# Kernel optimization log

Measured on AMD Instinct MI355X. Metric: run time of the kernel, lower is better.

Reference implementation:

```python
import jax, jax.numpy as jnp
import numpy as np

N_NODES = 50000
N_EDGES = 800000
IN_CH = 128
OUT_CH = 128


def setup_inputs() -> dict:
    key = jax.random.key(0)
    ks = jax.random.split(key, 8)
    x = jax.random.normal(ks[0], (N_NODES, IN_CH), dtype=jnp.float32)
    edge_index = jax.random.randint(ks[1], (2, N_EDGES), 0, N_NODES, dtype=jnp.int64)
    edge_weight = jax.random.uniform(ks[2], (N_EDGES,), dtype=jnp.float32)
    bound = 1.0 / np.sqrt(IN_CH)
    weight = jax.random.uniform(ks[3], (IN_CH, OUT_CH), minval=-bound, maxval=bound, dtype=jnp.float32)
    lin1_w = jax.random.uniform(ks[4], (OUT_CH, IN_CH), minval=-bound, maxval=bound, dtype=jnp.float32)
    lin1_b = jax.random.uniform(ks[5], (OUT_CH,), minval=-bound, maxval=bound, dtype=jnp.float32)
    lin2_w = jax.random.uniform(ks[6], (OUT_CH, IN_CH), minval=-bound, maxval=bound, dtype=jnp.float32)
    lin2_b = jax.random.uniform(ks[7], (OUT_CH,), minval=-bound, maxval=bound, dtype=jnp.float32)
    return {"x": x, "edge_index": edge_index, "edge_weight": edge_weight,
            "weight": weight, "lin1_w": lin1_w, "lin1_b": lin1_b,
            "lin2_w": lin2_w, "lin2_b": lin2_b}


def reference(x, edge_index, edge_weight, weight, lin1_w, lin1_b, lin2_w, lin2_b):
    num_nodes = x.shape[0]
    row, col = edge_index[0], edge_index[1]
    # remove_self_loops: zero out self-loop edge weights (equivalent math)
    ew = jnp.where(row == col, jnp.zeros((), x.dtype), edge_weight)
    h = x @ weight                                   # [N, out]
    deg = jax.ops.segment_sum(ew, row, num_segments=num_nodes)       # [N]
    h_j = ew[:, None] * h[col]                       # [E, out] gather + weight
    aggr_out = jax.ops.segment_sum(h_j, row, num_segments=num_nodes) # [N, out] scatter-add
    out = deg[:, None] * (x @ lin1_w.T + lin1_b) + aggr_out + (x @ lin2_w.T + lin2_b)
    return out
```

## Files before the change

kernel.cpp:

```cpp
#include <hip/hip_runtime.h>
#include <hip/hip_bf16.h>
#include <hip/hip_fp8.h>

#define NNODES 50000
#define NEDGES 800000
#define CH 128
#define NPAD 50176
#define NPART 256
#define RPP 196
#define PCAP 4096
#define BM 128

#define EPB1 4096
#define NB_PART ((NEDGES + EPB1 - 1) / EPB1)
#define BPS 200

#define NB_PREP 6250
#define NB_WCAT 256

typedef __attribute__((ext_vector_type(8))) short s8;
typedef __attribute__((ext_vector_type(4))) float f32x4;

__device__ inline unsigned pack_edge(int col, float w) {
    unsigned wb = __float_as_uint(w);
    return ((unsigned)col << 16) | ((wb + 0x4000u) >> 15);
}
__device__ inline float unpack_w(unsigned u) {
    return __uint_as_float((u & 0xFFFFu) << 15);
}

__global__ __launch_bounds__(256) void k_pre(const float* __restrict__ x,
                                             unsigned short* __restrict__ xb,
                                             unsigned char* __restrict__ xq,
                                             const float* __restrict__ weight,
                                             const float* __restrict__ l1,
                                             const float* __restrict__ l2,
                                             unsigned short* __restrict__ w1t,
                                             unsigned short* __restrict__ w2t,
                                             const int* __restrict__ ei,
                                             const float* __restrict__ ew,
                                             int* __restrict__ blkpack,
                                             int2* __restrict__ part) {
    const int blk = blockIdx.x;
    const int tid = threadIdx.x;
    if (blk < NB_PART) {
        __shared__ int hist[NPART];
        __shared__ int scn[NPART];
        __shared__ int wsum[4];
        __shared__ int2 stage[EPB1];
        const int lane = tid & 63, wid = tid >> 6;
        hist[tid] = 0;
        __syncthreads();
        const int e0 = blk * EPB1 + tid;
        int rows[16], cols[16], prt[16], rnk[16];
        float wv[16];
#pragma unroll
        for (int j = 0; j < 16; ++j) {
            int e = e0 + j * 256;
            bool v = (e < NEDGES);
            int ee = v ? e : 0;
            rows[j] = v ? ei[ee] : -1;
            cols[j] = ei[NEDGES + ee];
            wv[j] = ew[ee];
        }
#pragma unroll
        for (int j = 0; j < 16; ++j) {
            if (rows[j] >= 0) {
                prt[j] = rows[j] / RPP;
                rnk[j] = atomicAdd(&hist[prt[j]], 1);
            }
        }
        __syncthreads();
        int h = hist[tid];
        int s = h;
#pragma unroll
        for (int off = 1; off < 64; off <<= 1) {
            int u = __shfl_up(s, off);
            if (lane >= off) s += u;
        }
        if (lane == 63) wsum[wid] = s;
        __syncthreads();
        int base = 0;
#pragma unroll
        for (int w = 0; w < 4; ++w) if (w < wid) base += wsum[w];
        int excl = base + s - h;
        blkpack[tid * BPS + blk] = (excl << 13) | h;
        scn[tid] = excl;
        __syncthreads();
#pragma unroll
        for (int j = 0; j < 16; ++j) {
            if (rows[j] < 0) continue;
            int rl = rows[j] - prt[j] * RPP;
            float w = (rows[j] == cols[j]) ? 0.f : wv[j];
            stage[scn[prt[j]] + rnk[j]] =
                make_int2((rl << 16) | cols[j], __float_as_int(w));
        }
        __syncthreads();
        const int nblk = (NEDGES - blk * EPB1 < EPB1) ? (NEDGES - blk * EPB1) : EPB1;
        int2* dst = part + (size_t)blk * EPB1;
        for (int i = tid; i < nblk; i += 256) dst[i] = stage[i];
    } else if (blk < NB_PART + NB_PREP) {
        int g = (blk - NB_PART) * 256 + tid;
        float4 v = ((const float4*)x)[g];
        ushort4 o;
        __hip_bfloat16 b;
        b = __float2bfloat16(v.x); o.x = *(unsigned short*)&b;
        b = __float2bfloat16(v.y); o.y = *(unsigned short*)&b;
        b = __float2bfloat16(v.z); o.z = *(unsigned short*)&b;
        b = __float2bfloat16(v.w); o.w = *(unsigned short*)&b;
        ((ushort4*)xb)[g] = o;
        __hip_fp8_e4m3 q0(v.x), q1(v.y), q2(v.z), q3(v.w);
        uchar4 q;
        q.x = q0.__x; q.y = q1.__x; q.z = q2.__x; q.w = q3.__x;
        ((uchar4*)xq)[g] = q;
    } else {
        int c = blk - NB_PART - NB_PREP;
        int k = tid;
        if (c < CH) {
            if (k < CH) {
                __hip_bfloat16 b = __float2bfloat16(l1[c * CH + k]);
                w1t[(k >> 5) * 4096 + c * 32 + (k & 31)] = *(unsigned short*)&b;
            }
        } else {
            int cc = c - CH;
            float v = (k < CH) ? l2[cc * CH + k] : weight[(k - CH) * CH + cc];
            __hip_bfloat16 b = __float2bfloat16(v);
            w2t[(k >> 5) * 4096 + cc * 32 + (k & 31)] = *(unsigned short*)&b;
        }
    }
}

__global__ __launch_bounds__(256) void k_part2(const int* __restrict__ blkpack,
                                               const int2* __restrict__ part,
                                               unsigned* __restrict__ csr,
                                               int2* __restrict__ offlen) {
    __shared__ int dstoff[NPART + 1];
    __shared__ int b0a[NPART];
    __shared__ int wsum[4];
    __shared__ int rbase[NPART];
    __shared__ int rcur[NPART];
    __shared__ int2 sin[PCAP];
    __shared__ unsigned sout[PCAP];
    const int p = blockIdx.x;
    const int t = threadIdx.x;
    const int lane = t & 63, wid = t >> 6;

    int pk = (t < NB_PART) ? blkpack[p * BPS + t] : 0;
    int c = pk & 8191;
    b0a[t] = pk >> 13;
    rcur[t] = 0;
    int s = c;
#pragma unroll
    for (int off = 1; off < 64; off <<= 1) {
        int u = __shfl_up(s, off);
        if (lane >= off) s += u;
    }
    if (lane == 63) wsum[wid] = s;
    __syncthreads();
    int base = 0;
#pragma unroll
    for (int w = 0; w < 4; ++w) if (w < wid) base += wsum[w];
    int incl = base + s;
    dstoff[t] = incl - c;
    if (t == 255) dstoff[256] = incl;
    __syncthreads();
    int n = dstoff[256];
    if (n > PCAP) n = PCAP;

    for (int i = t; i < n; i += 256) {
        int lo = 0, hi = NPART - 1;
        while (lo < hi) {
            int mid = (lo + hi + 1) >> 1;
            if (dstoff[mid] <= i) lo = mid; else hi = mid - 1;
        }
        int2 eo = part[(size_t)lo * EPB1 + b0a[lo] + (i - dstoff[lo])];
        sin[i] = eo;
        atomicAdd(&rcur[((unsigned)eo.x) >> 16], 1);
    }
    __syncthreads();
    int rc = rcur[t];
    s = rc;
#pragma unroll
    for (int off = 1; off < 64; off <<= 1) {
        int u = __shfl_up(s, off);
        if (lane >= off) s += u;
    }
    if (lane == 63) wsum[wid] = s;
    __syncthreads();
    base = 0;
#pragma unroll
    for (int w = 0; w < 4; ++w) if (w < wid) base += wsum[w];
    rbase[t] = base + s - rc;
    rcur[t] = 0;
    __syncthreads();
    for (int i = t; i < n; i += 256) {
        int2 eo = sin[i];
        int rl = ((unsigned)eo.x) >> 16;
        int pos = rbase[rl] + atomicAdd(&rcur[rl], 1);
        sout[pos] = pack_edge(eo.x & 0xFFFF, __int_as_float(eo.y));
    }
    __syncthreads();
    const int gbase = p * PCAP;
    for (int i = t; i < n; i += 256) csr[gbase + i] = sout[i];
    if (t < RPP)
        offlen[p * RPP + t] = make_int2(gbase + rbase[t], rc);
}

__global__ __launch_bounds__(256) void k_agg(const int2* __restrict__ offlen,
                                             const unsigned* __restrict__ csr,
                                             const unsigned short* __restrict__ xq16,
                                             unsigned* __restrict__ xa2,
                                             float* __restrict__ deg) {
    const int node = blockIdx.x * 4 + (threadIdx.x >> 6);
    const int lane = threadIdx.x & 63;
    int2 ol = offlen[node];
    const unsigned* b = csr + ol.x;
    const int n = ol.y;
    float2 acc = make_float2(0.f, 0.f);
    float accw = 0.f;
    const int iters = (n + 7) >> 3;
    for (int it = 0; it < iters; ++it) {
        const int e0 = it * 8;
        unsigned u[8];
        unsigned short a[8];
        float wm[8];
#pragma unroll
        for (int j = 0; j < 8; ++j) {
            int idx = e0 + j;
            bool v = (idx < n);
            u[j] = b[v ? idx : 0];
            wm[j] = v ? 1.f : 0.f;
        }
#pragma unroll
        for (int j = 0; j < 8; ++j) a[j] = xq16[(size_t)(u[j] >> 16) * 64 + lane];
#pragma unroll
        for (int j = 0; j < 8; ++j) {
            float w = unpack_w(u[j]) * wm[j];
            __hip_fp8_e4m3 lo8, hi8;
            lo8.__x = (unsigned char)(a[j] & 0xff);
            hi8.__x = (unsigned char)(a[j] >> 8);
            float flo = (float)lo8, fhi = (float)hi8;
            accw += w;
            acc.x = fmaf(w, flo, acc.x);
            acc.y = fmaf(w, fhi, acc.y);
        }
    }
    __hip_bfloat16 lo = __float2bfloat16(acc.x);
    __hip_bfloat16 hi = __float2bfloat16(acc.y);
    unsigned u = (unsigned)(*(unsigned short*)&lo) | ((unsigned)(*(unsigned short*)&hi) << 16);
    xa2[(size_t)node * 64 + lane] = u;
    if (lane == 0) deg[node] = accw;
}

__global__ __launch_bounds__(512, 3) void k_gemm(const unsigned short* __restrict__ xb,
                                                 const unsigned short* __restrict__ xa,
                                                 const unsigned short* __restrict__ w1t,
                                                 const unsigned short* __restrict__ w2t,
                                                 const float* __restrict__ lin1_b,
                                                 const float* __restrict__ lin2_b,
                                                 const float* __restrict__ deg,
                                                 float* __restrict__ out) {
    __shared__ char bsm1[128 * 72];
    __shared__ char bsm2[128 * 72];

    const int tid = threadIdx.x;
    const int wid = tid >> 6;
    const int lane = tid & 63;
    const int brow = blockIdx.x * BM;
    const int arow = lane & 15;
    const int koff = (lane >> 4) * 8;

    int r = brow + wid * 16 + arow;
    r = (r < NNODES) ? r : (NNODES - 1);
    s8 af[8];
#pragma unroll
    for (int ks = 0; ks < 8; ++ks) {
        const unsigned short* ab = (ks < 4) ? xb : xa;
        af[ks] = *(const s8*)(ab + (size_t)r * CH + (ks & 3) * 32 + koff);
    }

    f32x4 acc[16];
#pragma unroll
    for (int t = 0; t < 16; ++t) acc[t] = (f32x4){0.f, 0.f, 0.f, 0.f};

#pragma unroll
    for (int ks = 0; ks < 8; ++ks) {
        __syncthreads();
        {
            const s8* src2 = (const s8*)(w2t + ks * 4096);
            int c = tid >> 2, prt = tid & 3;
            *(s8*)(bsm2 + c * 72 + prt * 16) = src2[tid];
            if (ks < 4) {
                const s8* src1 = (const s8*)(w1t + ks * 4096);
                *(s8*)(bsm1 + c * 72 + prt * 16) = src1[tid];
            }
        }
        __syncthreads();
        if (ks < 4) {
#pragma unroll
            for (int t = 0; t < 8; ++t) {
                s8 bf = *(const s8*)(bsm1 + (16 * t + arow) * 72 + koff * 2);
                acc[t] = __builtin_amdgcn_mfma_f32_16x16x32_bf16(bf, af[ks], acc[t], 0, 0, 0);
            }
        }
#pragma unroll
        for (int t = 0; t < 8; ++t) {
            s8 bf = *(const s8*)(bsm2 + (16 * t + arow) * 72 + koff * 2);
            acc[t + 8] = __builtin_amdgcn_mfma_f32_16x16x32_bf16(bf, af[ks], acc[t + 8], 0, 0, 0);
        }
    }

    const int row = brow + wid * 16 + (lane & 15);
    const int cg = (lane >> 4) * 4;
    if (row < NNODES) {
        const float dg = deg[row];
        float* orow = out + (size_t)row * CH;
#pragma unroll
        for (int t = 0; t < 8; ++t) {
            int c = 16 * t + cg;
            float4 b1 = *(const float4*)(lin1_b + c);
            float4 b2 = *(const float4*)(lin2_b + c);
            float4 o;
            o.x = dg * (acc[t][0] + b1.x) + (acc[t + 8][0] + b2.x);
            o.y = dg * (acc[t][1] + b1.y) + (acc[t + 8][1] + b2.y);
            o.z = dg * (acc[t][2] + b1.z) + (acc[t + 8][2] + b2.z);
            o.w = dg * (acc[t][3] + b1.w) + (acc[t + 8][3] + b2.w);
            *(float4*)(orow + c) = o;
        }
    }
}

extern "C" void kernel_launch(void* const* d_in, const int* in_sizes, int n_in,
                              void* d_out, int out_size, void* d_ws, size_t ws_size,
                              hipStream_t stream) {
    const float* x       = (const float*)d_in[0];
    const int*   ei      = (const int*)d_in[1];
    const float* ew      = (const float*)d_in[2];
    const float* weight  = (const float*)d_in[3];
    const float* lin1_w  = (const float*)d_in[4];
    const float* lin1_b  = (const float*)d_in[5];
    const float* lin2_w  = (const float*)d_in[6];
    const float* lin2_b  = (const float*)d_in[7];
    float* out = (float*)d_out;

    char* p = (char*)d_ws;
    unsigned short* xb  = (unsigned short*)p;    p += 12800000;
    unsigned char*  xq  = (unsigned char*)p;     p += 6400000;
    unsigned short* w1t = (unsigned short*)p;    p += 32768;
    unsigned short* w2t = (unsigned short*)p;    p += 65536;
    int*      blkpack = (int*)p;                 p += NPART * BPS * 4;
    float*    deg     = (float*)p;               p += NPAD * 4;
    int2*     offlen  = (int2*)p;                p += NPAD * 8;
    unsigned* csr     = (unsigned*)p;            p += (size_t)NPART * PCAP * 4;
    char* U = p;
    int2*           part = (int2*)U;
    unsigned short* xa   = (unsigned short*)U;

    k_pre<<<NB_PART + NB_PREP + NB_WCAT, 256, 0, stream>>>(x, xb, xq, weight, lin1_w,
                                                           lin2_w, w1t, w2t, ei, ew,
                                                           blkpack, part);
    k_part2<<<NPART, 256, 0, stream>>>(blkpack, part, csr, offlen);
    k_agg<<<NNODES / 4, 256, 0, stream>>>(offlen, csr, (const unsigned short*)xq,
                                          (unsigned*)xa, deg);
    k_gemm<<<NPAD / BM, 512, 0, stream>>>(xb, xa, w1t, w2t, lin1_b, lin2_b,
                                          deg, out);
}
```

Baseline: 78.29 us.

## Compact partition staging to packed edge plus row byte, widen part2 blocks

The partition pass now stores each edge as a pre-packed 32-bit col/weight word plus a separate 1-byte local row, replacing the 8-byte int2. This shrinks the intermediate traffic from 8 to 5 bytes per edge and moves the packing out of k_part2. k_part2 now runs 512 threads per block, with the scans still restricted to the first 256 threads. The x conversion blocks each handle two float4s per thread, so half as many blocks are launched. The tail copy of the row bytes uses uchar4 with nblk>>2, which drops remainder bytes when nblk is not a multiple of 4. The last block has 1280 edges, so this is safe here.

```diff
diff --git a/kernel.cpp b/kernel.cpp
--- a/kernel.cpp
+++ b/kernel.cpp
@@ -15,7 +15,7 @@
 #define NB_PART ((NEDGES + EPB1 - 1) / EPB1)
 #define BPS 200
 
-#define NB_PREP 6250
+#define NB_PREP 3125
 #define NB_WCAT 256
 
 typedef __attribute__((ext_vector_type(8))) short s8;
@@ -27,6 +27,23 @@
 }
 __device__ inline float unpack_w(unsigned u) {
     return __uint_as_float((u & 0xFFFFu) << 15);
+}
+
+__device__ inline void prep_one(const float* __restrict__ x,
+                                unsigned short* __restrict__ xb,
+                                unsigned char* __restrict__ xq, int g) {
+    float4 v = ((const float4*)x)[g];
+    ushort4 o;
+    __hip_bfloat16 b;
+    b = __float2bfloat16(v.x); o.x = *(unsigned short*)&b;
+    b = __float2bfloat16(v.y); o.y = *(unsigned short*)&b;
+    b = __float2bfloat16(v.z); o.z = *(unsigned short*)&b;
+    b = __float2bfloat16(v.w); o.w = *(unsigned short*)&b;
+    ((ushort4*)xb)[g] = o;
+    __hip_fp8_e4m3 q0(v.x), q1(v.y), q2(v.z), q3(v.w);
+    uchar4 q;
+    q.x = q0.__x; q.y = q1.__x; q.z = q2.__x; q.w = q3.__x;
+    ((uchar4*)xq)[g] = q;
 }
 
 __global__ __launch_bounds__(256) void k_pre(const float* __restrict__ x,
@@ -40,14 +57,16 @@
                                              const int* __restrict__ ei,
                                              const float* __restrict__ ew,
                                              int* __restrict__ blkpack,
-                                             int2* __restrict__ part) {
+                                             unsigned* __restrict__ partc,
+                                             unsigned char* __restrict__ partr) {
     const int blk = blockIdx.x;
     const int tid = threadIdx.x;
     if (blk < NB_PART) {
         __shared__ int hist[NPART];
         __shared__ int scn[NPART];
         __shared__ int wsum[4];
-        __shared__ int2 stage[EPB1];
+        __shared__ unsigned stgc[EPB1];
+        __shared__ unsigned char stgr[EPB1];
         const int lane = tid & 63, wid = tid >> 6;
         hist[tid] = 0;
         __syncthreads();
@@ -92,27 +111,21 @@
             if (rows[j] < 0) continue;
             int rl = rows[j] - prt[j] * RPP;
             float w = (rows[j] == cols[j]) ? 0.f : wv[j];
-            stage[scn[prt[j]] + rnk[j]] =
-                make_int2((rl << 16) | cols[j], __float_as_int(w));
+            int pos = scn[prt[j]] + rnk[j];
+            stgc[pos] = pack_edge(cols[j], w);
+            stgr[pos] = (unsigned char)rl;
         }
         __syncthreads();
         const int nblk = (NEDGES - blk * EPB1 < EPB1) ? (NEDGES - blk * EPB1) : EPB1;
-        int2* dst = part + (size_t)blk * EPB1;
-        for (int i = tid; i < nblk; i += 256) dst[i] = stage[i];
+        unsigned* dc = partc + (size_t)blk * EPB1;
+        for (int i = tid; i < nblk; i += 256) dc[i] = stgc[i];
+        uchar4* dr4 = (uchar4*)(partr + (size_t)blk * EPB1);
+        const uchar4* sr4 = (const uchar4*)stgr;
+        for (int i = tid; i < (nblk >> 2); i += 256) dr4[i] = sr4[i];
     } else if (blk < NB_PART + NB_PREP) {
-        int g = (blk - NB_PART) * 256 + tid;
-        float4 v = ((const float4*)x)[g];
-        ushort4 o;
-        __hip_bfloat16 b;
-        b = __float2bfloat16(v.x); o.x = *(unsigned short*)&b;
-        b = __float2bfloat16(v.y); o.y = *(unsigned short*)&b;
-        b = __float2bfloat16(v.z); o.z = *(unsigned short*)&b;
-        b = __float2bfloat16(v.w); o.w = *(unsigned short*)&b;
-        ((ushort4*)xb)[g] = o;
-        __hip_fp8_e4m3 q0(v.x), q1(v.y), q2(v.z), q3(v.w);
-        uchar4 q;
-        q.x = q0.__x; q.y = q1.__x; q.z = q2.__x; q.w = q3.__x;
-        ((uchar4*)xq)[g] = q;
+        int g = (blk - NB_PART) * 512 + tid;
+        prep_one(x, xb, xq, g);
+        prep_one(x, xb, xq, g + 256);
     } else {
         int c = blk - NB_PART - NB_PREP;
         int k = tid;
@@ -130,8 +143,9 @@
     }
 }
 
-__global__ __launch_bounds__(256) void k_part2(const int* __restrict__ blkpack,
-                                               const int2* __restrict__ part,
+__global__ __launch_bounds__(512) void k_part2(const int* __restrict__ blkpack,
+                                               const unsigned* __restrict__ partc,
+                                               const unsigned char* __restrict__ partr,
                                                unsigned* __restrict__ csr,
                                                int2* __restrict__ offlen) {
     __shared__ int dstoff[NPART + 1];
@@ -139,7 +153,8 @@
     __shared__ int wsum[4];
     __shared__ int rbase[NPART];
     __shared__ int rcur[NPART];
-    __shared__ int2 sin[PCAP];
+    __shared__ unsigned sc[PCAP];
+    __shared__ unsigned char sr[PCAP];
     __shared__ unsigned sout[PCAP];
     const int p = blockIdx.x;
     const int t = threadIdx.x;
@@ -147,61 +162,71 @@
 
     int pk = (t < NB_PART) ? blkpack[p * BPS + t] : 0;
     int c = pk & 8191;
-    b0a[t] = pk >> 13;
-    rcur[t] = 0;
     int s = c;
-#pragma unroll
-    for (int off = 1; off < 64; off <<= 1) {
-        int u = __shfl_up(s, off);
-        if (lane >= off) s += u;
-    }
-    if (lane == 63) wsum[wid] = s;
-    __syncthreads();
-    int base = 0;
-#pragma unroll
-    for (int w = 0; w < 4; ++w) if (w < wid) base += wsum[w];
-    int incl = base + s;
-    dstoff[t] = incl - c;
-    if (t == 255) dstoff[256] = incl;
+    if (t < 256) {
+        b0a[t] = pk >> 13;
+        rcur[t] = 0;
+#pragma unroll
+        for (int off = 1; off < 64; off <<= 1) {
+            int u = __shfl_up(s, off);
+            if (lane >= off) s += u;
+        }
+        if (lane == 63) wsum[wid] = s;
+    }
+    __syncthreads();
+    if (t < 256) {
+        int base = 0;
+#pragma unroll
+        for (int w = 0; w < 4; ++w) if (w < wid) base += wsum[w];
+        int incl = base + s;
+        dstoff[t] = incl - c;
+        if (t == 255) dstoff[256] = incl;
+    }
     __syncthreads();
     int n = dstoff[256];
     if (n > PCAP) n = PCAP;
 
-    for (int i = t; i < n; i += 256) {
+    for (int i = t; i < n; i += 512) {
         int lo = 0, hi = NPART - 1;
         while (lo < hi) {
             int mid = (lo + hi + 1) >> 1;
             if (dstoff[mid] <= i) lo = mid; else hi = mid - 1;
         }
-        int2 eo = part[(size_t)lo * EPB1 + b0a[lo] + (i - dstoff[lo])];
-        sin[i] = eo;
-        atomicAdd(&rcur[((unsigned)eo.x) >> 16], 1);
-    }
-    __syncthreads();
-    int rc = rcur[t];
-    s = rc;
-#pragma unroll
-    for (int off = 1; off < 64; off <<= 1) {
-        int u = __shfl_up(s, off);
-        if (lane >= off) s += u;
-    }
-    if (lane == 63) wsum[wid] = s;
-    __syncthreads();
-    base = 0;
-#pragma unroll
-    for (int w = 0; w < 4; ++w) if (w < wid) base += wsum[w];
-    rbase[t] = base + s - rc;
-    rcur[t] = 0;
-    __syncthreads();
-    for (int i = t; i < n; i += 256) {
-        int2 eo = sin[i];
-        int rl = ((unsigned)eo.x) >> 16;
+        size_t src = (size_t)lo * EPB1 + b0a[lo] + (i - dstoff[lo]);
+        unsigned cv = partc[src];
+        unsigned char rv = partr[src];
+        sc[i] = cv;
+        sr[i] = rv;
+        atomicAdd(&rcur[rv], 1);
+    }
+    __syncthreads();
+    int rc = (t < 256) ? rcur[t] : 0;
+    int s2 = rc;
+    if (t < 256) {
+#pragma unroll
+        for (int off = 1; off < 64; off <<= 1) {
+            int u = __shfl_up(s2, off);
+            if (lane >= off) s2 += u;
+        }
+        if (lane == 63) wsum[wid] = s2;
+    }
+    __syncthreads();
+    if (t < 256) {
+        int base = 0;
+#pragma unroll
+        for (int w = 0; w < 4; ++w) if (w < wid) base += wsum[w];
+        rbase[t] = base + s2 - rc;
+        rcur[t] = 0;
+    }
+    __syncthreads();
+    for (int i = t; i < n; i += 512) {
+        unsigned char rl = sr[i];
         int pos = rbase[rl] + atomicAdd(&rcur[rl], 1);
-        sout[pos] = pack_edge(eo.x & 0xFFFF, __int_as_float(eo.y));
+        sout[pos] = sc[i];
     }
     __syncthreads();
     const int gbase = p * PCAP;
-    for (int i = t; i < n; i += 256) csr[gbase + i] = sout[i];
+    for (int i = t; i < n; i += 512) csr[gbase + i] = sout[i];
     if (t < RPP)
         offlen[p * RPP + t] = make_int2(gbase + rbase[t], rc);
 }
@@ -353,13 +378,14 @@
     int2*     offlen  = (int2*)p;                p += NPAD * 8;
     unsigned* csr     = (unsigned*)p;            p += (size_t)NPART * PCAP * 4;
     char* U = p;
-    int2*           part = (int2*)U;
-    unsigned short* xa   = (unsigned short*)U;
+    unsigned*       partc = (unsigned*)U;
+    unsigned char*  partr = (unsigned char*)(U + (size_t)NB_PART * EPB1 * 4);
+    unsigned short* xa    = (unsigned short*)U;
 
     k_pre<<<NB_PART + NB_PREP + NB_WCAT, 256, 0, stream>>>(x, xb, xq, weight, lin1_w,
                                                            lin2_w, w1t, w2t, ei, ew,
-                                                           blkpack, part);
-    k_part2<<<NPART, 256, 0, stream>>>(blkpack, part, csr, offlen);
+                                                           blkpack, partc, partr);
+    k_part2<<<NPART, 512, 0, stream>>>(blkpack, partc, partr, csr, offlen);
     k_agg<<<NNODES / 4, 256, 0, stream>>>(offlen, csr, (const unsigned short*)xq,
                                           (unsigned*)xa, deg);
     k_gemm<<<NPAD / BM, 512, 0, stream>>>(xb, xa, w1t, w2t, lin1_b, lin2_b,
```

Measured after the change: 72.26 us, median of 2. 7.7% less time.
